# Optimization experiments

Measured on AMD Instinct MI355X. Metric: run time of the kernel, lower is better.

The kernel has to match this reference:

```python
import jax, jax.numpy as jnp
import numpy as np

B, S, H, NH = 2, 2048, 2048, 32
HD = H // NH  # 64

def _causal_mask(b, s, dtype=jnp.float32):
    neg = jnp.finfo(dtype).min
    m = jnp.where(jnp.tril(jnp.ones((s, s), dtype=bool)), 0.0, neg).astype(dtype)
    return jnp.broadcast_to(m[None, None], (b, 1, s, s))

def setup_inputs() -> dict:
    key = jax.random.key(0)
    k1, k2, k3, k4, k5 = jax.random.split(key, 5)
    scale = 1.0 / np.sqrt(H)
    return {
        "hidden_states": jax.random.normal(k1, (B, S, H), jnp.float32),
        "attention_mask": _causal_mask(B, S),
        "Wq": jax.random.normal(k2, (H, H), jnp.float32) * scale,
        "Wk": jax.random.normal(k3, (H, H), jnp.float32) * scale,
        "Wv": jax.random.normal(k4, (H, H), jnp.float32) * scale,
        "Wo": jax.random.normal(k5, (H, H), jnp.float32) * scale,
    }

def reference(hidden_states, attention_mask, Wq, Wk, Wv, Wo):
    b, s, _ = hidden_states.shape
    dt = hidden_states.dtype
    def proj(W):  # torch Linear: x @ W.T -> [b, nh, s, hd]
        return (hidden_states @ W.T).reshape(b, s, NH, HD).transpose(0, 2, 1, 3)
    q, k, v = proj(Wq), proj(Wk), proj(Wv)
    attn = jnp.einsum('bhqd,bhkd->bhqk', q, k) / np.sqrt(HD)
    attn = attn + attention_mask
    attn = jnp.maximum(attn, jnp.finfo(attn.dtype).min)
    attn = jax.nn.softmax(attn.astype(jnp.float32), axis=-1).astype(dt)
    out = jnp.einsum('bhqk,bhkd->bhqd', attn, v)
    out = out.transpose(0, 2, 1, 3).reshape(b, s, H)
    return out @ Wo.T
```

## Files before the change

### kernel.cpp

```cpp
#include <hip/hip_runtime.h>
#include <hip/hip_bf16.h>
#include <stdint.h>

#define S_LEN 2048
#define NHEAD 32
#define HDIM  64

using bf16x8 = __attribute__((ext_vector_type(8))) short;
using f32x4  = __attribute__((ext_vector_type(4))) float;
using f32x16 = __attribute__((ext_vector_type(16))) float;

__device__ __forceinline__ uint16_t f2bf(float f) {
  union { float f; uint32_t u; } c; c.f = f;
  uint32_t u = c.u;
  return (uint16_t)((u + 0x7FFFu + ((u >> 16) & 1u)) >> 16);
}

__device__ __forceinline__ void load_lds16(const void* g, void* l) {
  __builtin_amdgcn_global_load_lds(
      (const __attribute__((address_space(1))) void*)g,
      (__attribute__((address_space(3))) void*)l, 16, 0, 0);
}

__device__ __forceinline__ f32x16 mfma32(bf16x8 a, bf16x8 b, f32x16 c) {
  return __builtin_amdgcn_mfma_f32_32x32x16_bf16(a, b, c, 0, 0, 0);
}

__device__ __forceinline__ uint32_t cvtpk(float lo, float hi_) {
  uint32_t d;
  asm("v_cvt_pk_bf16_f32 %0, %1, %2" : "=v"(d) : "v"(lo), "v"(hi_));
  return d;
}
__device__ __forceinline__ void plswap(uint32_t& a, uint32_t& b) {
  asm volatile("v_permlane32_swap_b32 %0, %1" : "+v"(a), "+v"(b));
}

__global__ __launch_bounds__(256) void conv_batch(
    const float* __restrict__ X, const float* __restrict__ Wq,
    const float* __restrict__ Wk, const float* __restrict__ Wv,
    uint16_t* __restrict__ Xbf, uint16_t* __restrict__ Wqk,
    uint16_t* __restrict__ Wvb) {
  int i = blockIdx.x * 256 + threadIdx.x;
  const float* src; uint16_t* dst; int o;
  if (i < 2097152)      { src = X;  dst = Xbf;           o = i; }
  else if (i < 3145728) { src = Wq; dst = Wqk;           o = i - 2097152; }
  else if (i < 4194304) { src = Wk; dst = Wqk + 4194304; o = i - 3145728; }
  else                  { src = Wv; dst = Wvb;           o = i - 4194304; }
  float4 v = ((const float4*)src)[o];
  uint64_t packed = (uint64_t)f2bf(v.x) | ((uint64_t)f2bf(v.y) << 16) |
                    ((uint64_t)f2bf(v.z) << 32) | ((uint64_t)f2bf(v.w) << 48);
  ((uint64_t*)dst)[o] = packed;
}

__global__ __launch_bounds__(256) void conv_f32_bf16(
    const float* __restrict__ in, uint16_t* __restrict__ out, int n4) {
  int i = blockIdx.x * 256 + threadIdx.x;
  if (i < n4) {
    float4 v = ((const float4*)in)[i];
    uint64_t packed = (uint64_t)f2bf(v.x) | ((uint64_t)f2bf(v.y) << 16) |
                      ((uint64_t)f2bf(v.z) << 32) | ((uint64_t)f2bf(v.w) << 48);
    ((uint64_t*)out)[i] = packed;
  }
}

__global__ __launch_bounds__(256, 2) void gemm_qk(
    const uint16_t* __restrict__ A, const uint16_t* __restrict__ Bw,
    uint16_t* __restrict__ Qo, uint16_t* __restrict__ Ko, float qscale) {
  __shared__ __align__(16) char smem[2][24576];
  const int t = threadIdx.x;
  const int lane = t & 63, w = t >> 6;
  const int lrow = lane & 15, lgrp = lane >> 4;
  const int wm = (w >> 1) * 128, wn = (w & 1) * 64;
  const int id = blockIdx.x;
  const int xcd = id & 7, loc = id >> 3;
  const int bm = (loc & 15) * 256;
  const int bn = (xcd * 4 + (loc >> 4)) * 128;
  constexpr int NT = 2048 / 32;

  const f32x4 zero4 = {0.f, 0.f, 0.f, 0.f};
  f32x4 acc[8][4];
#pragma unroll
  for (int mi = 0; mi < 8; ++mi)
#pragma unroll
    for (int ni = 0; ni < 4; ++ni) acc[mi][ni] = zero4;

  auto stage = [&](char* buf, int kt) {
#pragma unroll
    for (int j = 0; j < 4; ++j) {
      const int s = t + j * 256;
      const int row = s >> 2;
      const int sc = (s & 3) ^ ((row >> 1) & 3);
      load_lds16(A + (size_t)(bm + row) * 2048 + kt + sc * 8,
                 buf + j * 4096 + w * 1024);
    }
#pragma unroll
    for (int j = 0; j < 2; ++j) {
      const int s = t + j * 256;
      const int row = s >> 2;
      const int sc = (s & 3) ^ ((row >> 1) & 3);
      load_lds16(Bw + (size_t)(bn + row) * 2048 + kt + sc * 8,
                 buf + 16384 + j * 4096 + w * 1024);
    }
  };
  auto ldf = [&](const char* base, int roff, int i) -> bf16x8 {
    const int row = roff + i * 16 + lrow;
    return *(const bf16x8*)(base + row * 64 +
                            ((lgrp ^ ((row >> 1) & 3)) << 4));
  };

  stage(smem[0], 0);
  stage(smem[1], 32);

  for (int kt = 0; kt < NT; ++kt) {
    char* cur = smem[kt & 1];
    if (kt < NT - 1) asm volatile("s_waitcnt vmcnt(6)" ::: "memory");
    else             asm volatile("s_waitcnt vmcnt(0)" ::: "memory");
    __builtin_amdgcn_s_barrier();

    bf16x8 aF[8], bF[4];
#pragma unroll
    for (int mi = 0; mi < 8; ++mi) aF[mi] = ldf(cur, wm, mi);
#pragma unroll
    for (int ni = 0; ni < 4; ++ni) bF[ni] = ldf(cur + 16384, wn, ni);
#pragma unroll
    for (int mi = 0; mi < 8; ++mi)
#pragma unroll
      for (int ni = 0; ni < 4; ++ni)
        acc[mi][ni] = __builtin_amdgcn_mfma_f32_16x16x32_bf16(
            aF[mi], bF[ni], acc[mi][ni], 0, 0, 0);

    __builtin_amdgcn_s_barrier();
    if (kt + 2 < NT) stage(cur, (kt + 2) * 32);
  }

  const bool isQ = (bn < 2048);
#pragma unroll
  for (int mi = 0; mi < 8; ++mi) {
#pragma unroll
    for (int ni = 0; ni < 4; ++ni) {
      const int n = bn + wn + ni * 16 + lrow;
      const int n2 = isQ ? n : (n - 2048);
      const int h = n2 >> 6, d = n2 & 63;
#pragma unroll
      for (int r = 0; r < 4; ++r) {
        const int m = bm + wm + mi * 16 + lgrp * 4 + r;
        const int b = m >> 11, s = m & 2047;
        const size_t off = (((size_t)(b * NHEAD + h) * S_LEN + s) * HDIM) + d;
        if (isQ) Qo[off] = f2bf(acc[mi][ni][r] * qscale);
        else     Ko[off] = f2bf(acc[mi][ni][r]);
      }
    }
  }
}

template<int MODE>
__global__ __launch_bounds__(256, 3) void gemm_nt(
    const uint16_t* __restrict__ A, const uint16_t* __restrict__ B,
    void* __restrict__ C, int M, int N, int K, float scale) {
  __shared__ __align__(16) char smem[3][16384];

  const int t = threadIdx.x;
  const int lane = t & 63, w = t >> 6;
  const int lrow = lane & 15, lgrp = lane >> 4;
  const int bm = blockIdx.y * 128, bn = blockIdx.x * 128;
  const int wm = (w >> 1) * 64, wn = (w & 1) * 64;
  const int NT = K / 32;

  const f32x4 zero4 = {0.f, 0.f, 0.f, 0.f};
  f32x4 acc[4][4];
#pragma unroll
  for (int mi = 0; mi < 4; ++mi)
#pragma unroll
    for (int ni = 0; ni < 4; ++ni) acc[mi][ni] = zero4;

  auto stage_mat = [&](const uint16_t* __restrict__ G, int grow0,
                       char* ldsbase, int kt) {
#pragma unroll
    for (int j = 0; j < 2; ++j) {
      const int s = t + j * 256;
      const int row = s >> 2;
      const int sc = (s & 3) ^ ((row >> 1) & 3);
      load_lds16(G + (size_t)(grow0 + row) * K + kt + sc * 8,
                 ldsbase + j * 4096 + w * 1024);
    }
  };
  auto ldf = [&](const char* Mb, int base, int i) -> bf16x8 {
    const int row = base + i * 16 + lrow;
    return *(const bf16x8*)(Mb + row * 64 + ((lgrp ^ ((row >> 1) & 3)) << 4));
  };

  stage_mat(A, bm, smem[0], 0);
  stage_mat(B, bn, smem[0] + 8192, 0);
  stage_mat(A, bm, smem[1], 32);
  stage_mat(B, bn, smem[1] + 8192, 32);

  for (int kt = 0; kt < NT; ++kt) {
    char* cur = smem[kt % 3];
    if (kt < NT - 1) asm volatile("s_waitcnt vmcnt(4)" ::: "memory");
    else             asm volatile("s_waitcnt vmcnt(0)" ::: "memory");
    __builtin_amdgcn_s_barrier();

    if (kt + 2 < NT) {
      char* nx2 = smem[(kt + 2) % 3];
      stage_mat(A, bm, nx2, (kt + 2) * 32);
      stage_mat(B, bn, nx2 + 8192, (kt + 2) * 32);
    }

    bf16x8 aF[4], bF[4];
#pragma unroll
    for (int mi = 0; mi < 4; ++mi) aF[mi] = ldf(cur, wm, mi);
#pragma unroll
    for (int ni = 0; ni < 4; ++ni) bF[ni] = ldf(cur + 8192, wn, ni);
#pragma unroll
    for (int mi = 0; mi < 4; ++mi)
#pragma unroll
      for (int ni = 0; ni < 4; ++ni)
        acc[mi][ni] = __builtin_amdgcn_mfma_f32_16x16x32_bf16(
            aF[mi], bF[ni], acc[mi][ni], 0, 0, 0);
  }

#pragma unroll
  for (int mi = 0; mi < 4; ++mi) {
#pragma unroll
    for (int ni = 0; ni < 4; ++ni) {
      const int n = bn + wn + ni * 16 + lrow;
#pragma unroll
      for (int r = 0; r < 4; ++r) {
        const int m = bm + wm + mi * 16 + lgrp * 4 + r;
        const float v = acc[mi][ni][r] * scale;
        if (MODE == 2) {
          ((float*)C)[(size_t)m * N + n] = v;
        } else {
          const int h = m >> 6, d = m & 63;
          const int b = n >> 11, s = n & 2047;
          ((uint16_t*)C)[(((size_t)(b * NHEAD + h) * HDIM + d) * S_LEN) + s] =
              f2bf(v);
        }
      }
    }
  }
}

__global__ __launch_bounds__(256, 3) void attn_kernel(
    const uint16_t* __restrict__ Q, const uint16_t* __restrict__ K,
    const uint16_t* __restrict__ Vt, uint16_t* __restrict__ O) {
  __shared__ __align__(16) uint16_t Ks[2][64 * 64];
  __shared__ __align__(16) uint16_t Vs[2][64 * 64];
  __shared__ float Ls[4][32];

  const int t = threadIdx.x, lane = t & 63, w = t >> 6;
  const int qcol = lane & 31, hi = lane >> 5;
  const int id = blockIdx.x;
  const int bh = (id & 7) * 8 + ((id >> 3) & 7);
  const int p = id >> 6;
  const int b = bh >> 5, h = bh & 31;

  const uint16_t* Qbh = Q + (size_t)bh * S_LEN * HDIM;
  const uint16_t* Kbh = K + (size_t)bh * S_LEN * HDIM;
  const uint16_t* Vbh = Vt + (size_t)bh * HDIM * S_LEN;

  const int srow = lane >> 3;
  const int schunk = (lane & 7) ^ srow;

  auto stage = [&](int k0, int bi) {
#pragma unroll
    for (int j = 0; j < 2; ++j) {
      const int r = j * 32 + w * 8 + srow;
      load_lds16(Kbh + (size_t)(k0 + r) * HDIM + schunk * 8,
                 (char*)&Ks[bi][0] + j * 4096 + w * 1024);
      load_lds16(Vbh + (size_t)r * S_LEN + k0 + schunk * 8,
                 (char*)&Vs[bi][0] + j * 4096 + w * 1024);
    }
  };

  for (int pass = 0; pass < 2; ++pass) {
    const int jq = pass ? (15 - p) : p;
    const int qw = jq * 128 + w * 32;
    const int qg = qw + qcol;

    bf16x8 qB[4];
    {
      const uint16_t* qp = Qbh + (size_t)(qw + qcol) * HDIM + hi * 8;
#pragma unroll
      for (int j = 0; j < 4; ++j) qB[j] = *(const bf16x8*)(qp + 16 * j);
    }

    f32x16 oacc0, oacc1;
#pragma unroll
    for (int r = 0; r < 16; ++r) { oacc0[r] = 0.f; oacc1[r] = 0.f; }
    float lsum = 0.f;

    const int nt = 2 * jq + 2;
    for (int kt = 0; kt < nt; ++kt) {
      const int cur = kt & 1;
      const int k0 = kt * 64;
      if (kt == 0) { __syncthreads(); stage(0, 0); }
      __syncthreads();
      if (kt + 1 < nt) stage((kt + 1) * 64, cur ^ 1);

      if (k0 <= qw + 31) {
        const char* Kc = (const char*)&Ks[cur][0];
        const char* Vc = (const char*)&Vs[cur][0];

        f32x16 s0, s1;
#pragma unroll
        for (int r = 0; r < 16; ++r) { s0[r] = 0.f; s1[r] = 0.f; }
        const int rk0 = qcol, rk1 = 32 + qcol;
        const int x0 = rk0 & 7;
        __builtin_amdgcn_s_setprio(1);
#pragma unroll
        for (int j = 0; j < 4; ++j) {
          bf16x8 kf0 = *(const bf16x8*)(Kc + rk0 * 128 + (((2*j+hi) ^ x0) << 4));
          bf16x8 kf1 = *(const bf16x8*)(Kc + rk1 * 128 + (((2*j+hi) ^ x0) << 4));
          s0 = mfma32(kf0, qB[j], s0);
          s1 = mfma32(kf1, qB[j], s1);
        }
        __builtin_amdgcn_s_setprio(0);

        if (k0 + 63 > qw) {
#pragma unroll
          for (int r = 0; r < 16; ++r) {
            const int krow = (r & 3) + 8 * (r >> 2) + 4 * hi;
            s0[r] = (k0 + krow <= qg) ? __expf(s0[r]) : 0.f;
            s1[r] = (k0 + 32 + krow <= qg) ? __expf(s1[r]) : 0.f;
            lsum += s0[r] + s1[r];
          }
        } else {
#pragma unroll
          for (int r = 0; r < 16; ++r) {
            s0[r] = __expf(s0[r]);
            s1[r] = __expf(s1[r]);
            lsum += s0[r] + s1[r];
          }
        }

        bf16x8 paf[4];
#pragma unroll
        for (int tt = 0; tt < 4; ++tt) {
          const int o = 8 * (tt & 1);
          uint32_t a0, a1, a2, a3;
          if (tt < 2) {
            a0 = cvtpk(s0[o + 0], s0[o + 1]);
            a1 = cvtpk(s0[o + 2], s0[o + 3]);
            a2 = cvtpk(s0[o + 4], s0[o + 5]);
            a3 = cvtpk(s0[o + 6], s0[o + 7]);
          } else {
            a0 = cvtpk(s1[o + 0], s1[o + 1]);
            a1 = cvtpk(s1[o + 2], s1[o + 3]);
            a2 = cvtpk(s1[o + 4], s1[o + 5]);
            a3 = cvtpk(s1[o + 6], s1[o + 7]);
          }
          plswap(a0, a2);
          plswap(a1, a3);
          union { uint32_t u[4]; bf16x8 v; } pk;
          pk.u[0] = a0; pk.u[1] = a1; pk.u[2] = a2; pk.u[3] = a3;
          paf[tt] = pk.v;
        }

        __builtin_amdgcn_s_setprio(1);
#pragma unroll
        for (int tt = 0; tt < 4; ++tt) {
          const int c = 2 * tt + hi;
          bf16x8 v0f = *(const bf16x8*)(Vc + rk0 * 128 + ((c ^ x0) << 4));
          bf16x8 v1f = *(const bf16x8*)(Vc + rk1 * 128 + ((c ^ x0) << 4));
          oacc0 = mfma32(paf[tt], v0f, oacc0);
          oacc1 = mfma32(paf[tt], v1f, oacc1);
        }
        __builtin_amdgcn_s_setprio(0);
      }
    }

    lsum += __shfl_xor(lsum, 32, 64);
    if (hi == 0) Ls[w][qcol] = 1.0f / lsum;

#pragma unroll
    for (int r = 0; r < 16; ++r) {
      const int qrow = (r & 3) + 8 * (r >> 2) + 4 * hi;
      const float inv = Ls[w][qrow];
      const size_t base = ((size_t)b * S_LEN + qw + qrow) * 2048 + h * 64;
      O[base + qcol] = f2bf(oacc0[r] * inv);
      O[base + 32 + qcol] = f2bf(oacc1[r] * inv);
    }
  }
}

extern "C" void kernel_launch(void* const* d_in, const int* in_sizes, int n_in,
                              void* d_out, int out_size, void* d_ws,
                              size_t ws_size, hipStream_t stream) {
  const float* X  = (const float*)d_in[0];
  const float* Wq = (const float*)d_in[2];
  const float* Wk = (const float*)d_in[3];
  const float* Wv = (const float*)d_in[4];
  const float* Wo = (const float*)d_in[5];
  float* out = (float*)d_out;

  char* ws = (char*)d_ws;
  uint16_t* Xbf = (uint16_t*)ws;
  uint16_t* Wqk = (uint16_t*)(ws + 16777216);
  uint16_t* Qb  = (uint16_t*)(ws + 33554432);
  uint16_t* Kb  = (uint16_t*)(ws + 50331648);
  uint16_t* Wsm = (uint16_t*)(ws + 67108864);
  uint16_t* Vtb = Wqk;
  uint16_t* Ob  = Xbf;

  const float qscale = 0.125f;

  conv_batch<<<20480, 256, 0, stream>>>(X, Wq, Wk, Wv, Xbf, Wqk, Wsm);
  gemm_qk<<<512, 256, 0, stream>>>(Xbf, Wqk, Qb, Kb, qscale);
  gemm_nt<1><<<dim3(32, 16), 256, 0, stream>>>(Wsm, Xbf, Vtb, 2048, 4096, 2048, 1.0f);
  attn_kernel<<<dim3(512), 256, 0, stream>>>(Qb, Kb, Vtb, Ob);
  conv_f32_bf16<<<4096, 256, 0, stream>>>(Wo, Wsm, 1048576);
  gemm_nt<2><<<dim3(16, 32), 256, 0, stream>>>(Ob, Wsm, out, 4096, 2048, 2048, 1.0f);
}
```

Measured before the change: 237.7 us.

## Load GEMM B fragments directly into registers, staging only A through LDS

In both the QK projection GEMM and the generic NT GEMM, the B operand tiles are no longer staged through LDS. Each lane now loads its MFMA B fragments straight from global memory into a register double-buffer, prefetched one k-tile ahead. LDS holds only A in a triple buffer, which shrinks shared memory use and removes the LDS reads for B and the extra barrier. The costs are duplicated global/L2 reads of B across waves, only one tile of latency hiding for B, and a lower occupancy hint (3 to 2) on gemm_nt.

```diff
diff --git a/kernel.cpp b/kernel.cpp
--- a/kernel.cpp
+++ b/kernel.cpp
@@ -66,7 +66,7 @@
 __global__ __launch_bounds__(256, 2) void gemm_qk(
     const uint16_t* __restrict__ A, const uint16_t* __restrict__ Bw,
     uint16_t* __restrict__ Qo, uint16_t* __restrict__ Ko, float qscale) {
-  __shared__ __align__(16) char smem[2][24576];
+  __shared__ __align__(16) char smem[3][16384];
   const int t = threadIdx.x;
   const int lane = t & 63, w = t >> 6;
   const int lrow = lane & 15, lgrp = lane >> 4;
@@ -84,7 +84,7 @@
 #pragma unroll
     for (int ni = 0; ni < 4; ++ni) acc[mi][ni] = zero4;
 
-  auto stage = [&](char* buf, int kt) {
+  auto stageA = [&](char* buf, int kt) {
 #pragma unroll
     for (int j = 0; j < 4; ++j) {
       const int s = t + j * 256;
@@ -93,45 +93,48 @@
       load_lds16(A + (size_t)(bm + row) * 2048 + kt + sc * 8,
                  buf + j * 4096 + w * 1024);
     }
-#pragma unroll
-    for (int j = 0; j < 2; ++j) {
-      const int s = t + j * 256;
-      const int row = s >> 2;
-      const int sc = (s & 3) ^ ((row >> 1) & 3);
-      load_lds16(Bw + (size_t)(bn + row) * 2048 + kt + sc * 8,
-                 buf + 16384 + j * 4096 + w * 1024);
-    }
   };
-  auto ldf = [&](const char* base, int roff, int i) -> bf16x8 {
-    const int row = roff + i * 16 + lrow;
-    return *(const bf16x8*)(base + row * 64 +
+  auto ldfA = [&](const char* buf, int mi) -> bf16x8 {
+    const int row = wm + mi * 16 + lrow;
+    return *(const bf16x8*)(buf + row * 64 +
                             ((lgrp ^ ((row >> 1) & 3)) << 4));
   };
-
-  stage(smem[0], 0);
-  stage(smem[1], 32);
-
-  for (int kt = 0; kt < NT; ++kt) {
-    char* cur = smem[kt & 1];
-    if (kt < NT - 1) asm volatile("s_waitcnt vmcnt(6)" ::: "memory");
-    else             asm volatile("s_waitcnt vmcnt(0)" ::: "memory");
-    __builtin_amdgcn_s_barrier();
-
-    bf16x8 aF[8], bF[4];
-#pragma unroll
-    for (int mi = 0; mi < 8; ++mi) aF[mi] = ldf(cur, wm, mi);
-#pragma unroll
-    for (int ni = 0; ni < 4; ++ni) bF[ni] = ldf(cur + 16384, wn, ni);
-#pragma unroll
-    for (int mi = 0; mi < 8; ++mi)
-#pragma unroll
-      for (int ni = 0; ni < 4; ++ni)
-        acc[mi][ni] = __builtin_amdgcn_mfma_f32_16x16x32_bf16(
-            aF[mi], bF[ni], acc[mi][ni], 0, 0, 0);
-
-    __builtin_amdgcn_s_barrier();
-    if (kt + 2 < NT) stage(cur, (kt + 2) * 32);
-  }
+  const uint16_t* Bbase = Bw + (size_t)(bn + wn + lrow) * 2048 + lgrp * 8;
+
+  bf16x8 bA[4], bB[4];
+  stageA(smem[0], 0);
+#pragma unroll
+  for (int ni = 0; ni < 4; ++ni) bA[ni] = *(const bf16x8*)(Bbase + ni * 32768);
+  stageA(smem[1], 32);
+
+#define QK_TILE(KT, BCUR, BNEXT)                                             \
+  {                                                                          \
+    if ((KT) < NT - 1) asm volatile("s_waitcnt vmcnt(4)" ::: "memory");      \
+    else               asm volatile("s_waitcnt vmcnt(0)" ::: "memory");      \
+    __builtin_amdgcn_s_barrier();                                            \
+    if ((KT) + 1 < NT) {                                                     \
+      _Pragma("unroll")                                                      \
+      for (int ni = 0; ni < 4; ++ni)                                         \
+        BNEXT[ni] = *(const bf16x8*)(Bbase + ni * 32768 + ((KT) + 1) * 32);  \
+    }                                                                        \
+    if ((KT) + 2 < NT) stageA(smem[((KT) + 2) % 3], ((KT) + 2) * 32);        \
+    const char* cur = smem[(KT) % 3];                                        \
+    bf16x8 aF[8];                                                            \
+    _Pragma("unroll")                                                        \
+    for (int mi = 0; mi < 8; ++mi) aF[mi] = ldfA(cur, mi);                   \
+    _Pragma("unroll")                                                        \
+    for (int mi = 0; mi < 8; ++mi)                                           \
+      _Pragma("unroll")                                                      \
+      for (int ni = 0; ni < 4; ++ni)                                         \
+        acc[mi][ni] = __builtin_amdgcn_mfma_f32_16x16x32_bf16(               \
+            aF[mi], BCUR[ni], acc[mi][ni], 0, 0, 0);                         \
+  }
+
+  for (int kt = 0; kt < NT; kt += 2) {
+    QK_TILE(kt, bA, bB);
+    QK_TILE(kt + 1, bB, bA);
+  }
+#undef QK_TILE
 
   const bool isQ = (bn < 2048);
 #pragma unroll
@@ -154,10 +157,10 @@
 }
 
 template<int MODE>
-__global__ __launch_bounds__(256, 3) void gemm_nt(
+__global__ __launch_bounds__(256, 2) void gemm_nt(
     const uint16_t* __restrict__ A, const uint16_t* __restrict__ B,
     void* __restrict__ C, int M, int N, int K, float scale) {
-  __shared__ __align__(16) char smem[3][16384];
+  __shared__ __align__(16) char smem[3][8192];
 
   const int t = threadIdx.x;
   const int lane = t & 63, w = t >> 6;
@@ -173,51 +176,58 @@
 #pragma unroll
     for (int ni = 0; ni < 4; ++ni) acc[mi][ni] = zero4;
 
-  auto stage_mat = [&](const uint16_t* __restrict__ G, int grow0,
-                       char* ldsbase, int kt) {
+  auto stageA = [&](char* buf, int kt) {
 #pragma unroll
     for (int j = 0; j < 2; ++j) {
       const int s = t + j * 256;
       const int row = s >> 2;
       const int sc = (s & 3) ^ ((row >> 1) & 3);
-      load_lds16(G + (size_t)(grow0 + row) * K + kt + sc * 8,
-                 ldsbase + j * 4096 + w * 1024);
+      load_lds16(A + (size_t)(bm + row) * K + kt + sc * 8,
+                 buf + j * 4096 + w * 1024);
     }
   };
-  auto ldf = [&](const char* Mb, int base, int i) -> bf16x8 {
-    const int row = base + i * 16 + lrow;
-    return *(const bf16x8*)(Mb + row * 64 + ((lgrp ^ ((row >> 1) & 3)) << 4));
+  auto ldfA = [&](const char* buf, int mi) -> bf16x8 {
+    const int row = wm + mi * 16 + lrow;
+    return *(const bf16x8*)(buf + row * 64 +
+                            ((lgrp ^ ((row >> 1) & 3)) << 4));
   };
-
-  stage_mat(A, bm, smem[0], 0);
-  stage_mat(B, bn, smem[0] + 8192, 0);
-  stage_mat(A, bm, smem[1], 32);
-  stage_mat(B, bn, smem[1] + 8192, 32);
-
-  for (int kt = 0; kt < NT; ++kt) {
-    char* cur = smem[kt % 3];
-    if (kt < NT - 1) asm volatile("s_waitcnt vmcnt(4)" ::: "memory");
-    else             asm volatile("s_waitcnt vmcnt(0)" ::: "memory");
-    __builtin_amdgcn_s_barrier();
-
-    if (kt + 2 < NT) {
-      char* nx2 = smem[(kt + 2) % 3];
-      stage_mat(A, bm, nx2, (kt + 2) * 32);
-      stage_mat(B, bn, nx2 + 8192, (kt + 2) * 32);
-    }
-
-    bf16x8 aF[4], bF[4];
-#pragma unroll
-    for (int mi = 0; mi < 4; ++mi) aF[mi] = ldf(cur, wm, mi);
-#pragma unroll
-    for (int ni = 0; ni < 4; ++ni) bF[ni] = ldf(cur + 8192, wn, ni);
-#pragma unroll
-    for (int mi = 0; mi < 4; ++mi)
-#pragma unroll
-      for (int ni = 0; ni < 4; ++ni)
-        acc[mi][ni] = __builtin_amdgcn_mfma_f32_16x16x32_bf16(
-            aF[mi], bF[ni], acc[mi][ni], 0, 0, 0);
-  }
+  const uint16_t* Bbase = B + (size_t)(bn + wn + lrow) * K + lgrp * 8;
+  const size_t bstep = (size_t)16 * K;
+
+  bf16x8 bA[4], bB[4];
+  stageA(smem[0], 0);
+#pragma unroll
+  for (int ni = 0; ni < 4; ++ni) bA[ni] = *(const bf16x8*)(Bbase + ni * bstep);
+  stageA(smem[1], 32);
+
+#define NT_TILE(KT, BCUR, BNEXT)                                             \
+  {                                                                          \
+    if ((KT) < NT - 1) asm volatile("s_waitcnt vmcnt(2)" ::: "memory");      \
+    else               asm volatile("s_waitcnt vmcnt(0)" ::: "memory");      \
+    __builtin_amdgcn_s_barrier();                                            \
+    if ((KT) + 1 < NT) {                                                     \
+      _Pragma("unroll")                                                      \
+      for (int ni = 0; ni < 4; ++ni)                                         \
+        BNEXT[ni] = *(const bf16x8*)(Bbase + ni * bstep + ((KT) + 1) * 32);  \
+    }                                                                        \
+    if ((KT) + 2 < NT) stageA(smem[((KT) + 2) % 3], ((KT) + 2) * 32);        \
+    const char* cur = smem[(KT) % 3];                                        \
+    bf16x8 aF[4];                                                            \
+    _Pragma("unroll")                                                        \
+    for (int mi = 0; mi < 4; ++mi) aF[mi] = ldfA(cur, mi);                   \
+    _Pragma("unroll")                                                        \
+    for (int mi = 0; mi < 4; ++mi)                                           \
+      _Pragma("unroll")                                                      \
+      for (int ni = 0; ni < 4; ++ni)                                         \
+        acc[mi][ni] = __builtin_amdgcn_mfma_f32_16x16x32_bf16(               \
+            aF[mi], BCUR[ni], acc[mi][ni], 0, 0, 0);                         \
+  }
+
+  for (int kt = 0; kt < NT; kt += 2) {
+    NT_TILE(kt, bA, bB);
+    NT_TILE(kt + 1, bB, bA);
+  }
+#undef NT_TILE
 
 #pragma unroll
   for (int mi = 0; mi < 4; ++mi) {
```

New measurement: 327.3 us. 37.7% more time.
